# Kernel optimization log

Hardware: AMD Instinct MI355X
Metric: run time of the kernel (lower is better)

Reference implementation:

```python
import jax, jax.numpy as jnp
import numpy as np

D = 1024   # hidden
H = 4      # heads
HD = D // H
E = 8      # experts
FF = 4096  # expert ffn dim
CAP_FACTOR = 1.0


def _ln(x, g, b, eps=1e-5):
    mu = jnp.mean(x, -1, keepdims=True)
    v = jnp.mean((x - mu) ** 2, -1, keepdims=True)
    return (x - mu) * jax.lax.rsqrt(v + eps) * g + b


def setup_inputs() -> dict:
    key = jax.random.key(0)
    ks = jax.random.split(key, 8)
    L, N = 1024, 16
    s = 0.02
    return {
        "x": jax.random.normal(ks[0], (L, N, D), jnp.float32),
        "in_proj_w": jax.random.normal(ks[1], (3 * D, D), jnp.float32) * s,
        "in_proj_b": jnp.zeros((3 * D,), jnp.float32),
        "out_proj_w": jax.random.normal(ks[2], (D, D), jnp.float32) * s,
        "out_proj_b": jnp.zeros((D,), jnp.float32),
        "ln1_g": jnp.ones((D,), jnp.float32),
        "ln1_b": jnp.zeros((D,), jnp.float32),
        "ln2_g": jnp.ones((D,), jnp.float32),
        "ln2_b": jnp.zeros((D,), jnp.float32),
        "wg": jax.random.normal(ks[3], (D, E), jnp.float32) * s,
        "w1": jax.random.normal(ks[4], (E, D, FF), jnp.float32) * s,
        "b1": jnp.zeros((E, FF), jnp.float32),
        "w2": jax.random.normal(ks[5], (E, FF, D), jnp.float32) * s,
        "b2": jnp.zeros((E, D), jnp.float32),
    }


def _mha(x, w, b, ow, ob):
    # x: [L, N, D] (torch MultiheadAttention layout, batch_first=False)
    L, N, _ = x.shape
    qkv = x @ w.T + b
    q, k, v = jnp.split(qkv, 3, axis=-1)
    rh = lambda t: t.reshape(L, N, H, HD).transpose(1, 2, 0, 3)  # -> [N,H,L,HD]
    q, k, v = rh(q), rh(k), rh(v)
    scores = jnp.einsum('nhld,nhmd->nhlm', q, k) / np.float32(np.sqrt(HD))
    attn = jax.nn.softmax(scores, axis=-1)
    o = jnp.einsum('nhlm,nhmd->nhld', attn, v).transpose(2, 0, 1, 3).reshape(L, N, D)
    return o @ ow.T + ob


def _moe(x, wg, w1, b1, w2, b2):
    # top-1 switch gating with capacity drop, dispatch, grouped GEMM, combine
    L, N, _ = x.shape
    S = L * N
    cap = int(CAP_FACTOR * S) // E  # 2048
    xf = x.reshape(S, D)
    gates = jax.nn.softmax(xf @ wg, axis=-1)           # [S,E]
    idx = jnp.argmax(gates, axis=-1)                    # [S] top-1 expert
    mask1 = jax.nn.one_hot(idx, E, dtype=x.dtype)       # [S,E]
    # position of each token within its expert's queue
    loc = jnp.sum((jnp.cumsum(mask1, 0) - 1.0) * mask1, -1).astype(jnp.int32)
    keep = loc < cap                                    # capacity drop mask
    gate_val = jnp.take_along_axis(gates, idx[:, None], -1)[:, 0]
    slot = jnp.where(keep, idx.astype(jnp.int32) * cap + loc, E * cap)  # OOB if dropped
    disp = jnp.zeros((E * cap, D), x.dtype).at[slot].set(xf, mode='drop')
    disp = disp.reshape(E, cap, D)
    # expert = Linear(D,FF) -> Linear(FF,D), NO activation between (per source)
    h = jnp.einsum('ecd,edf->ecf', disp, w1) + b1[:, None, :]
    y = (jnp.einsum('ecf,efd->ecd', h, w2) + b2[:, None, :]).reshape(E * cap, D)
    out = jnp.where(keep[:, None], gate_val[:, None] * y[jnp.minimum(slot, E * cap - 1)], 0.0)
    return out.reshape(L, N, D)


def reference(x, in_proj_w, in_proj_b, out_proj_w, out_proj_b,
              ln1_g, ln1_b, ln2_g, ln2_b, wg, w1, b1, w2, b2):
    y1 = _ln(x + _mha(x, in_proj_w, in_proj_b, out_proj_w, out_proj_b), ln1_g, ln1_b)
    y2 = _ln(y1 + _moe(y1, wg, w1, b1, w2, b2), ln2_g, ln2_b)
    return y2
```

## Files before the change

### kernel.cpp

```cpp
#include <hip/hip_runtime.h>
#include <hip/hip_bf16.h>

typedef __bf16 bf16_t;
typedef bf16_t bf16x4 __attribute__((ext_vector_type(4)));
typedef bf16_t bf16x8 __attribute__((ext_vector_type(8)));
typedef float  f32x4  __attribute__((ext_vector_type(4)));
typedef _Float16 half4 __attribute__((ext_vector_type(4)));
typedef _Float16 half8 __attribute__((ext_vector_type(8)));

#define L_  1024
#define N_  16
#define S_  16384
#define D_  1024
#define H_  4
#define HD_ 256
#define E_  8
#define FF_ 4096
#define CAP_ 2048
#define ESLOTS_ (E_*CAP_)
#define TAU_ 0.03f

__device__ __forceinline__ void gload16(const void* g, void* l) {
  __builtin_amdgcn_global_load_lds(
      (const __attribute__((address_space(1))) void*)g,
      (__attribute__((address_space(3))) void*)l,
      16, 0, 0);
}

#define SRC_SWZ(lane) (((lane) & 3) ^ (((lane) >> 3) & 3))

__global__ __launch_bounds__(256) void split2(
    const float* __restrict__ in, _Float16* __restrict__ oh,
    _Float16* __restrict__ ol, long n4)
{
  long i = (long)blockIdx.x * blockDim.x + threadIdx.x;
  long stride = (long)gridDim.x * blockDim.x;
  for (; i < n4; i += stride) {
    float4 v = ((const float4*)in)[i];
    half4 h, l;
    h.x = (_Float16)v.x; l.x = (_Float16)((v.x - (float)h.x) * 4096.0f);
    h.y = (_Float16)v.y; l.y = (_Float16)((v.y - (float)h.y) * 4096.0f);
    h.z = (_Float16)v.z; l.z = (_Float16)((v.z - (float)h.z) * 4096.0f);
    h.w = (_Float16)v.w; l.w = (_Float16)((v.w - (float)h.w) * 4096.0f);
    ((half4*)oh)[i] = h;
    ((half4*)ol)[i] = l;
  }
}

template<int EPI, bool HAS_BIAS, int PROD>
__global__ __launch_bounds__(256) void hgemm3s(
    const _Float16* __restrict__ Ah, const _Float16* __restrict__ Al,
    const _Float16* __restrict__ Bh, const _Float16* __restrict__ Bl,
    float* __restrict__ Cf, _Float16* __restrict__ Ch, _Float16* __restrict__ Cl,
    const float* __restrict__ bias,
    int K, long lda, long ldb, long ldcf, long ldch,
    int Z2, long sA1, long sA2, long sB1, long sB2, long sC1, long sC2, long sBias)
{
  constexpr int NL = (PROD == 3) ? 2 : 1;
  __shared__ _Float16 tA[NL][2][128 * 32];
  __shared__ _Float16 tB[NL][2][64 * 32];
  const int z  = blockIdx.z;
  const int z1 = z / Z2, z2 = z - z1 * Z2;
  const long aoff = (long)z1 * sA1 + (long)z2 * sA2;
  const long boff = (long)z1 * sB1 + (long)z2 * sB2;
  const long coff = (long)z1 * sC1 + (long)z2 * sC2;
  const int brow = blockIdx.y * 128, bcol = blockIdx.x * 64;
  const int tid = threadIdx.x, lane = tid & 63, wid = tid >> 6;
  const int wr = (wid >> 1) * 64, wc = (wid & 1) * 32;
  const int fr = lane & 15;
  const int fqs = (((lane >> 4) ^ ((fr >> 1) & 3)) * 8);

  const bool isA = (wid < 2);
  int limb, dstoff, nch;
  const _Float16* ssrc;
  if constexpr (PROD == 3) {
    limb = wid & 1; nch = isA ? 8 : 4; dstoff = 0;
    ssrc = (wid == 0) ? Ah : (wid == 1) ? Al : (wid == 2) ? Bh : Bl;
  } else {
    limb = 0; nch = isA ? 4 : 2; dstoff = (wid & 1) * nch;
    ssrc = isA ? Ah : Bh;
  }
  const long sld = isA ? lda : ldb;
  const long soff = isA ? aoff : boff;
  int srow = (isA ? brow : bcol) + (lane >> 2);
  if constexpr (PROD == 1) srow += (wid & 1) * (isA ? 64 : 32);
  const _Float16* sbase = ssrc + soff + (long)srow * sld + SRC_SWZ(lane) * 8;

  f32x4 acc0[4][2], acc1[4][2];
#pragma unroll
  for (int mi = 0; mi < 4; ++mi)
#pragma unroll
    for (int ni = 0; ni < 2; ++ni) {
      acc0[mi][ni] = f32x4{0.f, 0.f, 0.f, 0.f};
      acc1[mi][ni] = f32x4{0.f, 0.f, 0.f, 0.f};
    }

  {
    _Float16* d0 = (isA ? &tA[limb][0][0] : &tB[limb][0][0]) + dstoff * 512;
    for (int i = 0; i < nch; ++i)
      gload16(sbase + (long)(16 * i) * sld, d0 + i * 512);
  }
  __syncthreads();

  const int NT = K >> 5;
  for (int t = 0; t < NT; ++t) {
    const int cur = t & 1;
    if (t + 1 < NT) {
      const int k1 = (t + 1) * 32;
      _Float16* d0 = (isA ? &tA[limb][cur ^ 1][0] : &tB[limb][cur ^ 1][0]) + dstoff * 512;
      for (int i = 0; i < nch; ++i)
        gload16(sbase + (long)(16 * i) * sld + k1, d0 + i * 512);
    }

    half8 bh_[2], bl_[2];
#pragma unroll
    for (int ni = 0; ni < 2; ++ni) {
      bh_[ni] = *(const half8*)&tB[0][cur][(wc + ni * 16 + fr) * 32 + fqs];
      if constexpr (PROD == 3)
        bl_[ni] = *(const half8*)&tB[1][cur][(wc + ni * 16 + fr) * 32 + fqs];
    }
    half8 ah_[4], al_[4];
#pragma unroll
    for (int mi = 0; mi < 4; ++mi) {
      ah_[mi] = *(const half8*)&tA[0][cur][(wr + mi * 16 + fr) * 32 + fqs];
      if constexpr (PROD == 3)
        al_[mi] = *(const half8*)&tA[1][cur][(wr + mi * 16 + fr) * 32 + fqs];
    }
#pragma unroll
    for (int mi = 0; mi < 4; ++mi)
#pragma unroll
      for (int ni = 0; ni < 2; ++ni)
        acc0[mi][ni] = __builtin_amdgcn_mfma_f32_16x16x32_f16(ah_[mi], bh_[ni], acc0[mi][ni], 0, 0, 0);
    if constexpr (PROD == 3) {
#pragma unroll
      for (int mi = 0; mi < 4; ++mi)
#pragma unroll
        for (int ni = 0; ni < 2; ++ni)
          acc1[mi][ni] = __builtin_amdgcn_mfma_f32_16x16x32_f16(ah_[mi], bl_[ni], acc1[mi][ni], 0, 0, 0);
#pragma unroll
      for (int mi = 0; mi < 4; ++mi)
#pragma unroll
        for (int ni = 0; ni < 2; ++ni)
          acc1[mi][ni] = __builtin_amdgcn_mfma_f32_16x16x32_f16(al_[mi], bh_[ni], acc1[mi][ni], 0, 0, 0);
    }
    __syncthreads();
  }

#pragma unroll
  for (int mi = 0; mi < 4; ++mi) {
#pragma unroll
    for (int ni = 0; ni < 2; ++ni) {
      int gcol = bcol + wc + ni * 16 + fr;
      float bv = 0.0f;
      if constexpr (HAS_BIAS) bv = bias[(long)z1 * sBias + gcol];
#pragma unroll
      for (int v = 0; v < 4; ++v) {
        int grow = brow + wr + mi * 16 + (lane >> 4) * 4 + v;
        float val = acc0[mi][ni][v] + bv;
        if constexpr (PROD == 3) val += acc1[mi][ni][v] * 0.000244140625f;
        if constexpr (EPI == 0) {
          Cf[coff + (long)grow * ldcf + gcol] = val;
        } else if constexpr (EPI == 1) {
          _Float16 hh = (_Float16)val;
          _Float16 ll = (_Float16)((val - (float)hh) * 4096.0f);
          long ci = coff + (long)grow * ldch + gcol;
          Ch[ci] = hh; Cl[ci] = ll;
        } else if constexpr (EPI == 3) {
          Ch[coff + (long)grow * ldch + gcol] = (_Float16)val;
        } else {
          if (bcol < 2048) {
            _Float16 hh = (_Float16)val;
            _Float16 ll = (_Float16)((val - (float)hh) * 4096.0f);
            long ci = (long)grow * ldch + gcol;
            Ch[ci] = hh; Cl[ci] = ll;
          } else {
            Cf[(long)grow * ldcf + (gcol - 2048)] = val;
          }
        }
      }
    }
  }
}

template<bool OUT_BF16, bool HAS_BIAS>
__global__ __launch_bounds__(256) void bgemm16(
    const bf16_t* __restrict__ A, const bf16_t* __restrict__ B,
    void* __restrict__ Cout, const float* __restrict__ bias,
    int K, long lda, long ldb, long ldc,
    long sA1, long sB1, long sC1, long sBias)
{
  __shared__ bf16_t tiles[2][2][128 * 32];
  const int z = blockIdx.z;
  const long coff = (long)z * sC1;
  const int brow = blockIdx.y * 128, bcol = blockIdx.x * 128;
  const int tid = threadIdx.x, lane = tid & 63, wid = tid >> 6;
  const int wr = (wid >> 1) * 64, wc = (wid & 1) * 64;
  const int fr = lane & 15;
  const int fqs = (((lane >> 4) ^ ((fr >> 1) & 3)) * 8);

  const bf16_t* src0 = (wid < 2) ? (A + (long)z * sA1) : (B + (long)z * sB1);
  const long ld = (wid < 2) ? lda : ldb;
  const int  rb = ((wid < 2) ? brow : bcol) + 64 * (wid & 1) + (lane >> 2);
  const bf16_t* srcbase = src0 + (long)rb * ld + SRC_SWZ(lane) * 8;
  const int tsel = wid >> 1, halfsel = wid & 1;

  f32x4 acc[4][4];
#pragma unroll
  for (int mi = 0; mi < 4; ++mi)
#pragma unroll
    for (int ni = 0; ni < 4; ++ni)
      acc[mi][ni] = f32x4{0.0f, 0.0f, 0.0f, 0.0f};

#pragma unroll
  for (int i = 0; i < 4; ++i)
    gload16(srcbase + (long)(16 * i) * ld, &tiles[tsel][0][(4 * halfsel + i) * 512]);
  __syncthreads();

  const int NT = K >> 5;
  for (int t = 0; t < NT; ++t) {
    const int cur = t & 1;
    if (t + 1 < NT) {
      const int k1 = (t + 1) * 32;
#pragma unroll
      for (int i = 0; i < 4; ++i)
        gload16(srcbase + (long)(16 * i) * ld + k1, &tiles[tsel][cur ^ 1][(4 * halfsel + i) * 512]);
    }
    bf16x8 af[4], bfv[4];
#pragma unroll
    for (int i = 0; i < 4; ++i) {
      af[i]  = *(const bf16x8*)&tiles[0][cur][(wr + i * 16 + fr) * 32 + fqs];
      bfv[i] = *(const bf16x8*)&tiles[1][cur][(wc + i * 16 + fr) * 32 + fqs];
    }
#pragma unroll
    for (int mi = 0; mi < 4; ++mi)
#pragma unroll
      for (int ni = 0; ni < 4; ++ni)
        acc[mi][ni] = __builtin_amdgcn_mfma_f32_16x16x32_bf16(af[mi], bfv[ni], acc[mi][ni], 0, 0, 0);
    __syncthreads();
  }

#pragma unroll
  for (int mi = 0; mi < 4; ++mi) {
#pragma unroll
    for (int ni = 0; ni < 4; ++ni) {
      int gcol = bcol + wc + ni * 16 + fr;
      float bv = 0.0f;
      if constexpr (HAS_BIAS) bv = bias[(long)z * sBias + gcol];
#pragma unroll
      for (int v = 0; v < 4; ++v) {
        int grow = brow + wr + mi * 16 + (lane >> 4) * 4 + v;
        float val = acc[mi][ni][v] + bv;
        long ci = coff + (long)grow * ldc + gcol;
        if constexpr (OUT_BF16) ((bf16_t*)Cout)[ci] = (bf16_t)val;
        else                    ((float*)Cout)[ci]  = val;
      }
    }
  }
}

template<typename TOUT>
__global__ __launch_bounds__(256) void transpose_f32(
    const float* __restrict__ src, TOUT* __restrict__ dst,
    long ld_src, long ld_dst, int Z2,
    long ss1, long ss2, long sd1, long sd2)
{
  __shared__ float t[32][33];
  const int z = blockIdx.z, z1 = z / Z2, z2 = z - z1 * Z2;
  src += (long)z1 * ss1 + (long)z2 * ss2;
  dst += (long)z1 * sd1 + (long)z2 * sd2;
  const int c0 = blockIdx.x * 32, r0 = blockIdx.y * 32;
  const int tx = threadIdx.x & 31, ty = threadIdx.x >> 5;
#pragma unroll
  for (int i = 0; i < 4; ++i)
    t[ty + i * 8][tx] = src[(long)(r0 + ty + i * 8) * ld_src + c0 + tx];
  __syncthreads();
#pragma unroll
  for (int i = 0; i < 4; ++i)
    dst[(long)(c0 + ty + i * 8) * ld_dst + r0 + tx] = (TOUT)t[tx][ty + i * 8];
}

__global__ __launch_bounds__(256) void transpose_split(
    const float* __restrict__ src, _Float16* __restrict__ dh, _Float16* __restrict__ dl,
    long ld_src, long ld_dst, int Z2,
    long ss1, long ss2, long sd1, long sd2)
{
  __shared__ float t[32][33];
  const int z = blockIdx.z, z1 = z / Z2, z2 = z - z1 * Z2;
  src += (long)z1 * ss1 + (long)z2 * ss2;
  dh  += (long)z1 * sd1 + (long)z2 * sd2;
  dl  += (long)z1 * sd1 + (long)z2 * sd2;
  const int c0 = blockIdx.x * 32, r0 = blockIdx.y * 32;
  const int tx = threadIdx.x & 31, ty = threadIdx.x >> 5;
#pragma unroll
  for (int i = 0; i < 4; ++i)
    t[ty + i * 8][tx] = src[(long)(r0 + ty + i * 8) * ld_src + c0 + tx];
  __syncthreads();
#pragma unroll
  for (int i = 0; i < 4; ++i) {
    float v = t[tx][ty + i * 8];
    _Float16 h = (_Float16)v;
    _Float16 l = (_Float16)((v - (float)h) * 4096.0f);
    long idx = (long)(c0 + ty + i * 8) * ld_dst + r0 + tx;
    dh[idx] = h;
    dl[idx] = l;
  }
}

template<bool WRITE_LO>
__global__ __launch_bounds__(256) void softmax_pack(
    float* __restrict__ Sm, float scale)
{
  __shared__ float red[4];
  const long row = blockIdx.x;
  const float4* p = (const float4*)(Sm + row * 1024);
  const int tid = threadIdx.x;
  float4 v = p[tid];
  float m = fmaxf(fmaxf(v.x, v.y), fmaxf(v.z, v.w));
#pragma unroll
  for (int o = 32; o; o >>= 1) m = fmaxf(m, __shfl_xor(m, o, 64));
  if ((tid & 63) == 0) red[tid >> 6] = m;
  __syncthreads();
  m = fmaxf(fmaxf(red[0], red[1]), fmaxf(red[2], red[3]));
  __syncthreads();
  float e0 = __expf((v.x - m) * scale);
  float e1 = __expf((v.y - m) * scale);
  float e2 = __expf((v.z - m) * scale);
  float e3 = __expf((v.w - m) * scale);
  float s = e0 + e1 + e2 + e3;
#pragma unroll
  for (int o = 32; o; o >>= 1) s += __shfl_xor(s, o, 64);
  if ((tid & 63) == 0) red[tid >> 6] = s;
  __syncthreads();
  s = red[0] + red[1] + red[2] + red[3];
  float inv = 1.0f / s;
  float p0 = e0 * inv, p1 = e1 * inv, p2 = e2 * inv, p3 = e3 * inv;
  half4 h;
  h.x = (_Float16)p0; h.y = (_Float16)p1; h.z = (_Float16)p2; h.w = (_Float16)p3;
  _Float16* base = (_Float16*)Sm + row * 2048;
  ((half4*)base)[tid] = h;
  if constexpr (WRITE_LO) {
    half4 l;
    l.x = (_Float16)((p0 - (float)h.x) * 4096.0f);
    l.y = (_Float16)((p1 - (float)h.y) * 4096.0f);
    l.z = (_Float16)((p2 - (float)h.z) * 4096.0f);
    l.w = (_Float16)((p3 - (float)h.w) * 4096.0f);
    ((half4*)(base + 1024))[tid] = l;
  }
}

__global__ __launch_bounds__(256) void add_ln_gate(
    const float* __restrict__ x, const float* __restrict__ attn,
    const float* __restrict__ g, const float* __restrict__ be,
    const float* __restrict__ wg, bf16_t* __restrict__ yb,
    int* __restrict__ idx, float* __restrict__ gval,
    int* __restrict__ bcnt16, int* __restrict__ blist16)
{
  __shared__ float red[4];
  __shared__ float lred[4][8];
  const long s = blockIdx.x;
  const int tid = threadIdx.x;
  const int lane = tid & 63, w = tid >> 6;
  float4 va = ((const float4*)(x + s * 1024))[tid];
  float4 vb = ((const float4*)(attn + s * 1024))[tid];
  float v0 = va.x + vb.x, v1 = va.y + vb.y, v2 = va.z + vb.z, v3 = va.w + vb.w;
  float sum = v0 + v1 + v2 + v3;
#pragma unroll
  for (int o = 32; o; o >>= 1) sum += __shfl_xor(sum, o, 64);
  if (lane == 0) red[w] = sum;
  __syncthreads();
  float mu = (red[0] + red[1] + red[2] + red[3]) * (1.0f / 1024.0f);
  __syncthreads();
  float d0 = v0 - mu, d1 = v1 - mu, d2 = v2 - mu, d3 = v3 - mu;
  float ss = d0 * d0 + d1 * d1 + d2 * d2 + d3 * d3;
#pragma unroll
  for (int o = 32; o; o >>= 1) ss += __shfl_xor(ss, o, 64);
  if (lane == 0) red[w] = ss;
  __syncthreads();
  float var = (red[0] + red[1] + red[2] + red[3]) * (1.0f / 1024.0f);
  float rstd = rsqrtf(var + 1e-5f);
  float4 vg  = ((const float4*)g)[tid];
  float4 vbe = ((const float4*)be)[tid];
  float y0 = d0 * rstd * vg.x + vbe.x;
  float y1v = d1 * rstd * vg.y + vbe.y;
  float y2v = d2 * rstd * vg.z + vbe.z;
  float y3 = d3 * rstd * vg.w + vbe.w;
  bf16x4 ov = { (bf16_t)y0, (bf16_t)y1v, (bf16_t)y2v, (bf16_t)y3 };
  *(bf16x4*)(yb + s * 1024 + tid * 4) = ov;
  float lg[8];
  const float* w0 = wg + (long)(tid * 4) * 8;
#pragma unroll
  for (int e = 0; e < 8; ++e)
    lg[e] = y0 * w0[e] + y1v * w0[8 + e] + y2v * w0[16 + e] + y3 * w0[24 + e];
#pragma unroll
  for (int e = 0; e < 8; ++e) {
#pragma unroll
    for (int o = 32; o; o >>= 1) lg[e] += __shfl_xor(lg[e], o, 64);
  }
  if (lane == 0) {
#pragma unroll
    for (int e = 0; e < 8; ++e) lred[w][e] = lg[e];
  }
  __syncthreads();
  if (tid == 0) {
    float Lg[8];
#pragma unroll
    for (int e = 0; e < 8; ++e)
      Lg[e] = lred[0][e] + lred[1][e] + lred[2][e] + lred[3][e];
    float best = Lg[0], second = -1e30f; int bi = 0;
#pragma unroll
    for (int e = 1; e < 8; ++e) {
      if (Lg[e] > best) { second = best; best = Lg[e]; bi = e; }
      else if (Lg[e] > second) second = Lg[e];
    }
    float sm = 0.0f;
#pragma unroll
    for (int e = 0; e < 8; ++e) sm += __expf(Lg[e] - best);
    idx[s] = bi;
    gval[s] = 1.0f / sm;
    if (best - second < TAU_) {
      int n = (int)(s & 15);
      int p = atomicAdd(&bcnt16[n], 1);
      if (p < 128) blist16[n * 128 + p] = (int)s;
    }
  }
}

__global__ void zero16(int* __restrict__ p)
{
  if (threadIdx.x < 16) p[threadIdx.x] = 0;
}

__global__ __launch_bounds__(64) void qp_gather(
    const int* __restrict__ bcnt16, const int* __restrict__ blist16,
    const _Float16* __restrict__ QKh, const _Float16* __restrict__ QKl,
    _Float16* __restrict__ Qph, _Float16* __restrict__ Qpl)
{
  const int b = blockIdx.x;
  const int n = b >> 7, p = b & 127;
  const int t = threadIdx.x;
  half8* dh = (half8*)(Qph + (long)b * 1024);
  half8* dl = (half8*)(Qpl + (long)b * 1024);
  int cnt = bcnt16[n]; if (cnt > 128) cnt = 128;
  if (p < cnt) {
    long srow = (long)blist16[b] * 2048;
    const half8* sh = (const half8*)(QKh + srow);
    const half8* sl = (const half8*)(QKl + srow);
    dh[t * 2]     = sh[t * 2];
    dh[t * 2 + 1] = sh[t * 2 + 1];
    dl[t * 2]     = sl[t * 2];
    dl[t * 2 + 1] = sl[t * 2 + 1];
  } else {
    half8 z;
#pragma unroll
    for (int i = 0; i < 8; ++i) z[i] = (_Float16)0.0f;
    dh[t * 2] = z; dh[t * 2 + 1] = z;
    dl[t * 2] = z; dl[t * 2 + 1] = z;
  }
}

__global__ __launch_bounds__(256) void gate_fix(
    const int* __restrict__ bcnt16, const int* __restrict__ blist16,
    const float* __restrict__ attn_p, const float* __restrict__ x,
    const float* __restrict__ g, const float* __restrict__ be,
    const float* __restrict__ wg,
    int* __restrict__ idx, float* __restrict__ gval)
{
  const int b = blockIdx.x;
  const int n = b >> 7, p = b & 127;
  int cnt = bcnt16[n]; if (cnt > 128) cnt = 128;
  if (p >= cnt) return;
  const long s = blist16[b];
  __shared__ float red[4];
  __shared__ float lred[4][8];
  const int tid = threadIdx.x;
  const int lane = tid & 63, w = tid >> 6;
  float4 va = ((const float4*)(x + s * 1024))[tid];
  float4 vb = ((const float4*)(attn_p + (long)b * 1024))[tid];
  float v0 = va.x + vb.x, v1 = va.y + vb.y, v2 = va.z + vb.z, v3 = va.w + vb.w;
  float sum = v0 + v1 + v2 + v3;
#pragma unroll
  for (int o = 32; o; o >>= 1) sum += __shfl_xor(sum, o, 64);
  if (lane == 0) red[w] = sum;
  __syncthreads();
  float mu = (red[0] + red[1] + red[2] + red[3]) * (1.0f / 1024.0f);
  __syncthreads();
  float d0 = v0 - mu, d1 = v1 - mu, d2 = v2 - mu, d3 = v3 - mu;
  float ss = d0 * d0 + d1 * d1 + d2 * d2 + d3 * d3;
#pragma unroll
  for (int o = 32; o; o >>= 1) ss += __shfl_xor(ss, o, 64);
  if (lane == 0) red[w] = ss;
  __syncthreads();
  float var = (red[0] + red[1] + red[2] + red[3]) * (1.0f / 1024.0f);
  float rstd = rsqrtf(var + 1e-5f);
  float4 vg  = ((const float4*)g)[tid];
  float4 vbe = ((const float4*)be)[tid];
  float y0 = d0 * rstd * vg.x + vbe.x;
  float y1v = d1 * rstd * vg.y + vbe.y;
  float y2v = d2 * rstd * vg.z + vbe.z;
  float y3 = d3 * rstd * vg.w + vbe.w;
  float lg[8];
  const float* w0 = wg + (long)(tid * 4) * 8;
#pragma unroll
  for (int e = 0; e < 8; ++e)
    lg[e] = y0 * w0[e] + y1v * w0[8 + e] + y2v * w0[16 + e] + y3 * w0[24 + e];
#pragma unroll
  for (int e = 0; e < 8; ++e) {
#pragma unroll
    for (int o = 32; o; o >>= 1) lg[e] += __shfl_xor(lg[e], o, 64);
  }
  if (lane == 0) {
#pragma unroll
    for (int e = 0; e < 8; ++e) lred[w][e] = lg[e];
  }
  __syncthreads();
  if (tid == 0) {
    float Lg[8];
#pragma unroll
    for (int e = 0; e < 8; ++e)
      Lg[e] = lred[0][e] + lred[1][e] + lred[2][e] + lred[3][e];
    float best = Lg[0]; int bi = 0;
#pragma unroll
    for (int e = 1; e < 8; ++e) { if (Lg[e] > best) { best = Lg[e]; bi = e; } }
    float sm = 0.0f;
#pragma unroll
    for (int e = 0; e < 8; ++e) sm += __expf(Lg[e] - best);
    idx[s] = bi;
    gval[s] = 1.0f / sm;
  }
}

__global__ __launch_bounds__(256) void combine_ln(
    const bf16_t* __restrict__ y1b, const bf16_t* __restrict__ ymoe,
    const int* __restrict__ slot, const float* __restrict__ gval,
    const float* __restrict__ g, const float* __restrict__ be,
    float* __restrict__ out)
{
  __shared__ float red[4];
  const long s = blockIdx.x;
  const int tid = threadIdx.x;
  const int lane = tid & 63, w = tid >> 6;
  int sl = slot[s];
  bool keep = sl < ESLOTS_;
  float gv = keep ? gval[s] : 0.0f;
  long mrow = keep ? (long)sl * 1024 : 0;
  bf16x4 ya = *(const bf16x4*)(y1b + s * 1024 + tid * 4);
  bf16x4 ym = *(const bf16x4*)(ymoe + mrow + tid * 4);
  float v0 = (float)ya[0] + gv * (float)ym[0];
  float v1 = (float)ya[1] + gv * (float)ym[1];
  float v2 = (float)ya[2] + gv * (float)ym[2];
  float v3 = (float)ya[3] + gv * (float)ym[3];
  float sum = v0 + v1 + v2 + v3;
#pragma unroll
  for (int o = 32; o; o >>= 1) sum += __shfl_xor(sum, o, 64);
  if (lane == 0) red[w] = sum;
  __syncthreads();
  float mu = (red[0] + red[1] + red[2] + red[3]) * (1.0f / 1024.0f);
  __syncthreads();
  float d0 = v0 - mu, d1 = v1 - mu, d2 = v2 - mu, d3 = v3 - mu;
  float ss = d0 * d0 + d1 * d1 + d2 * d2 + d3 * d3;
#pragma unroll
  for (int o = 32; o; o >>= 1) ss += __shfl_xor(ss, o, 64);
  if (lane == 0) red[w] = ss;
  __syncthreads();
  float var = (red[0] + red[1] + red[2] + red[3]) * (1.0f / 1024.0f);
  float rstd = rsqrtf(var + 1e-5f);
  float4 vg  = ((const float4*)g)[tid];
  float4 vbe = ((const float4*)be)[tid];
  float4 ov = {d0 * rstd * vg.x + vbe.x, d1 * rstd * vg.y + vbe.y,
               d2 * rstd * vg.z + vbe.z, d3 * rstd * vg.w + vbe.w};
  ((float4*)(out + s * 1024))[tid] = ov;
}

__global__ __launch_bounds__(1024) void route_scan(
    const int* __restrict__ idx, int* __restrict__ slot, int* __restrict__ tfs)
{
  __shared__ int c_lds[8][1024];
  const int tid = threadIdx.x;
  const int lane = tid & 63, wid = tid >> 6;

  for (int j = tid; j < ESLOTS_; j += 1024) tfs[j] = -1;

  int myc[8] = {0, 0, 0, 0, 0, 0, 0, 0};
  for (int j = 0; j < 16; ++j) {
    int e = idx[tid * 16 + j];
    myc[e]++;
  }
#pragma unroll
  for (int e = 0; e < 8; ++e) c_lds[e][tid] = myc[e];
  __syncthreads();

  if (wid < 8) {
    int carry = 0;
    for (int cb = 0; cb < 1024; cb += 64) {
      int v = c_lds[wid][cb + lane];
#pragma unroll
      for (int o = 1; o < 64; o <<= 1) {
        int t = __shfl_up(v, o, 64);
        if (lane >= o) v += t;
      }
      v += carry;
      c_lds[wid][cb + lane] = v;
      carry = __shfl(v, 63, 64);
    }
  }
  __syncthreads();

  int run[8] = {0, 0, 0, 0, 0, 0, 0, 0};
  for (int j = 0; j < 16; ++j) {
    int s = tid * 16 + j;
    int e = idx[s];
    int excl = c_lds[e][tid] - myc[e];
    int loc = excl + run[e];
    run[e]++;
    int sl = (loc < CAP_) ? e * CAP_ + loc : ESLOTS_;
    slot[s] = sl;
    if (sl < ESLOTS_) tfs[sl] = s;
  }
}

__global__ void dispatch_rows(
    const int* __restrict__ tfs, const bf16_t* __restrict__ y1b,
    bf16_t* __restrict__ disp)
{
  const int row = blockIdx.x;
  const int t = tfs[row];
  bf16x8* d = (bf16x8*)(disp + (long)row * 1024);
  if (t >= 0) {
    const bf16x8* sp = (const bf16x8*)(y1b + (long)t * 1024);
    d[threadIdx.x] = sp[threadIdx.x];
  } else {
    bf16x8 zv;
#pragma unroll
    for (int i = 0; i < 8; ++i) zv[i] = (bf16_t)0.0f;
    d[threadIdx.x] = zv;
  }
}

__global__ void fill_val(float* __restrict__ p, float v, long n)
{
  long i = (long)blockIdx.x * blockDim.x + threadIdx.x;
  long stride = (long)gridDim.x * blockDim.x;
  for (; i < n; i += stride) p[i] = v;
}

extern "C" void kernel_launch(void* const* d_in, const int* in_sizes, int n_in,
                              void* d_out, int out_size, void* d_ws, size_t ws_size,
                              hipStream_t stream)
{
  const float* x    = (const float*)d_in[0];
  const float* Wqkv = (const float*)d_in[1];
  const float* bqkv = (const float*)d_in[2];
  const float* Wo   = (const float*)d_in[3];
  const float* bo   = (const float*)d_in[4];
  const float* g1   = (const float*)d_in[5];
  const float* b1n  = (const float*)d_in[6];
  const float* g2   = (const float*)d_in[7];
  const float* b2n  = (const float*)d_in[8];
  const float* wg   = (const float*)d_in[9];
  const float* w1   = (const float*)d_in[10];
  const float* b1e  = (const float*)d_in[11];
  const float* w2   = (const float*)d_in[12];
  const float* b2e  = (const float*)d_in[13];
  float* out = (float*)d_out;

  const size_t MB = 1ull << 20;
  const size_t REQUIRED = 384 * MB;
  if (ws_size < REQUIRED) {
    fill_val<<<2048, 256, 0, stream>>>(out, (float)(ws_size >> 20), (long)out_size);
    return;
  }

  char* ws = (char*)d_ws;
  _Float16* Xh   = (_Float16*)(ws + 0);
  _Float16* Xl   = (_Float16*)(ws + 32 * MB);
  _Float16* Wqh  = (_Float16*)(ws + 64 * MB);
  _Float16* Wql  = (_Float16*)(ws + 70 * MB);
  float*    scores = (float*)(ws + 0);
  _Float16* Woh  = (_Float16*)(ws + 64 * MB);
  _Float16* Wol  = (_Float16*)(ws + 66 * MB);
  _Float16* QKh  = (_Float16*)(ws + 80 * MB);
  _Float16* QKl  = (_Float16*)(ws + 144 * MB);
  float*    Vf32 = (float*)(ws + 208 * MB);
  _Float16* oh   = (_Float16*)(ws + 208 * MB);
  _Float16* vTh  = (_Float16*)(ws + 272 * MB);
  _Float16* vTl  = (_Float16*)(ws + 304 * MB);
  float*    attn = (float*)(ws + 0);
  bf16_t*   y1b  = (bf16_t*)(ws + 208 * MB);
  float*    scp   = (float*)(ws + 0);
  _Float16* Qph   = (_Float16*)(ws + 32 * MB);
  _Float16* Qpl   = (_Float16*)(ws + 36 * MB);
  _Float16* o_ph  = (_Float16*)(ws + 40 * MB);
  _Float16* o_pl  = (_Float16*)(ws + 44 * MB);
  float*    attnp = (float*)(ws + 48 * MB);
  int*      idx  = (int*)(ws + 336 * MB);
  int*      slot = idx + S_;
  float*    gval = (float*)(slot + S_);
  int*      tfs  = (int*)(gval + S_);
  int*      bcnt16  = tfs + S_;
  int*      blist16 = bcnt16 + 16;
  bf16_t*   disp = (bf16_t*)(ws + 272 * MB);
  bf16_t*   W1t  = (bf16_t*)(ws + 0);
  bf16_t*   W2t  = (bf16_t*)(ws + 0);
  bf16_t*   h    = (bf16_t*)(ws + 80 * MB);
  bf16_t*   ymoe = (bf16_t*)(ws + 304 * MB);

  zero16<<<1, 64, 0, stream>>>(bcnt16);

  split2<<<4096, 256, 0, stream>>>(x, Xh, Xl, (long)S_ * D_ / 4);
  split2<<<2048, 256, 0, stream>>>(Wqkv, Wqh, Wql, (long)3 * D_ * D_ / 4);

  hgemm3s<2, true, 3><<<dim3(48, 128, 1), 256, 0, stream>>>(
      Xh, Xl, Wqh, Wql, Vf32, QKh, QKl, bqkv,
      D_, D_, D_, D_, 2 * D_,
      1, 0, 0, 0, 0, 0, 0, 0);

  split2<<<1024, 256, 0, stream>>>(Wo, Woh, Wol, (long)D_ * D_ / 4);

  transpose_split<<<dim3(HD_ / 32, L_ / 32, 64), 256, 0, stream>>>(
      Vf32, vTh, vTl, (long)N_ * D_, L_,
      H_, D_, HD_, (long)H_ * HD_ * L_, (long)HD_ * L_);

  for (int g = 0; g < 4; ++g) {
    const long qko = (long)g * 4 * 2048;
    hgemm3s<0, false, 1><<<dim3(16, 8, 16), 256, 0, stream>>>(
        QKh + qko, QKl + qko, QKh + qko + 1024, QKl + qko + 1024,
        scores, nullptr, nullptr, nullptr,
        HD_, (long)N_ * 2048, (long)N_ * 2048, L_, 0,
        H_, 2048, 256, 2048, 256, (long)H_ * L_ * L_, (long)L_ * L_, 0);
    softmax_pack<false><<<4 * H_ * L_, 256, 0, stream>>>(scores, 0.0625f);
    hgemm3s<3, false, 1><<<dim3(4, 8, 16), 256, 0, stream>>>(
        (_Float16*)scores, (_Float16*)scores + 1024,
        vTh + (long)g * 4 * H_ * HD_ * L_, vTl + (long)g * 4 * H_ * HD_ * L_,
        nullptr, oh + (long)g * 4 * D_, nullptr, nullptr,
        L_, 2048, L_, 0, (long)N_ * D_,
        H_, (long)4 * L_ * 2048, (long)L_ * 2048,
        (long)H_ * HD_ * L_, (long)HD_ * L_, D_, HD_, 0);
  }

  hgemm3s<0, true, 1><<<dim3(16, 128, 1), 256, 0, stream>>>(
      oh, nullptr, Woh, Wol, attn, nullptr, nullptr, bo,
      D_, D_, D_, D_, 0,
      1, 0, 0, 0, 0, 0, 0, 0);

  add_ln_gate<<<S_, 256, 0, stream>>>(x, attn, g1, b1n, wg, y1b,
                                      idx, gval, bcnt16, blist16);

  qp_gather<<<2048, 64, 0, stream>>>(bcnt16, blist16, QKh, QKl, Qph, Qpl);
  hgemm3s<0, false, 3><<<dim3(16, 1, 64), 256, 0, stream>>>(
      Qph, Qpl, QKh + 1024, QKl + 1024, scp, nullptr, nullptr, nullptr,
      HD_, 1024, (long)N_ * 2048, 1024, 0,
      4, (long)128 * 1024, 256, 2048, 256,
      (long)4 * 128 * 1024, (long)128 * 1024, 0);
  softmax_pack<true><<<64 * 128, 256, 0, stream>>>(scp, 0.0625f);
  hgemm3s<1, false, 3><<<dim3(4, 1, 64), 256, 0, stream>>>(
      (_Float16*)scp, (_Float16*)scp + 1024, vTh, vTl,
      nullptr, o_ph, o_pl, nullptr,
      L_, 2048, L_, 0, 1024,
      4, (long)4 * 128 * 2048, (long)128 * 2048,
      (long)H_ * HD_ * L_, (long)HD_ * L_,
      (long)128 * 1024, 256, 0);
  hgemm3s<0, true, 3><<<dim3(16, 16, 1), 256, 0, stream>>>(
      o_ph, o_pl, Woh, Wol, attnp, nullptr, nullptr, bo,
      D_, D_, D_, D_, 0,
      1, 0, 0, 0, 0, 0, 0, 0);
  gate_fix<<<2048, 256, 0, stream>>>(bcnt16, blist16, attnp, x,
                                     g1, b1n, wg, idx, gval);

  route_scan<<<1, 1024, 0, stream>>>(idx, slot, tfs);

  dispatch_rows<<<ESLOTS_, 128, 0, stream>>>(tfs, y1b, disp);

  transpose_f32<bf16_t><<<dim3(FF_ / 32, D_ / 32, E_), 256, 0, stream>>>(
      w1, W1t, FF_, D_, 1, (long)D_ * FF_, 0, (long)FF_ * D_, 0);

  bgemm16<true, true><<<dim3(32, 16, 8), 256, 0, stream>>>(
      disp, W1t, h, b1e, D_, D_, D_, FF_,
      (long)CAP_ * D_, (long)FF_ * D_, (long)CAP_ * FF_, FF_);

  transpose_f32<bf16_t><<<dim3(D_ / 32, FF_ / 32, E_), 256, 0, stream>>>(
      w2, W2t, D_, FF_, 1, (long)FF_ * D_, 0, (long)D_ * FF_, 0);

  bgemm16<true, true><<<dim3(8, 16, 8), 256, 0, stream>>>(
      h, W2t, ymoe, b2e, FF_, FF_, FF_, D_,
      (long)CAP_ * FF_, (long)D_ * FF_, (long)CAP_ * D_, D_);

  combine_ln<<<S_, 256, 0, stream>>>(y1b, ymoe, slot, gval, g2, b2n, out);
}
```

Baseline: 1.610 ms.

## Use 256x128 MoE GEMM tiles and single-fp16 attention scores with fewer passes

The expert GEMM kernel now uses 512-thread blocks covering 256x128 output tiles. Each warp loads three 16-row chunks into separate A and B shared tiles, so more output is computed per B-tile load. Attention scores are now written directly as fp16 by the QK GEMM and normalised in place by a new fp16 softmax. The PV GEMM then reads only the high half, not a hi/lo split pair. Batches double to cut the loop to two groups, which lowers score memory traffic and launch count at some cost in precision of the attention probabilities.

```diff
diff --git a/kernel.cpp b/kernel.cpp
--- a/kernel.cpp
+++ b/kernel.cpp
@@ -183,26 +183,41 @@
 }
 
 template<bool OUT_BF16, bool HAS_BIAS>
-__global__ __launch_bounds__(256) void bgemm16(
+__global__ __launch_bounds__(512) void bgemm256(
     const bf16_t* __restrict__ A, const bf16_t* __restrict__ B,
     void* __restrict__ Cout, const float* __restrict__ bias,
     int K, long lda, long ldb, long ldc,
     long sA1, long sB1, long sC1, long sBias)
 {
-  __shared__ bf16_t tiles[2][2][128 * 32];
+  __shared__ bf16_t tA[2][256 * 32];
+  __shared__ bf16_t tB[2][128 * 32];
   const int z = blockIdx.z;
   const long coff = (long)z * sC1;
-  const int brow = blockIdx.y * 128, bcol = blockIdx.x * 128;
+  const int brow = blockIdx.y * 256, bcol = blockIdx.x * 128;
   const int tid = threadIdx.x, lane = tid & 63, wid = tid >> 6;
   const int wr = (wid >> 1) * 64, wc = (wid & 1) * 64;
   const int fr = lane & 15;
   const int fqs = (((lane >> 4) ^ ((fr >> 1) & 3)) * 8);
 
-  const bf16_t* src0 = (wid < 2) ? (A + (long)z * sA1) : (B + (long)z * sB1);
-  const long ld = (wid < 2) ? lda : ldb;
-  const int  rb = ((wid < 2) ? brow : bcol) + 64 * (wid & 1) + (lane >> 2);
-  const bf16_t* srcbase = src0 + (long)rb * ld + SRC_SWZ(lane) * 8;
-  const int tsel = wid >> 1, halfsel = wid & 1;
+  const bf16_t* Ab = A + (long)z * sA1;
+  const bf16_t* Bb = B + (long)z * sB1;
+
+  const bf16_t* csrc[3];
+  bf16_t* cd0[3];
+  bf16_t* cd1[3];
+  long cld[3];
+#pragma unroll
+  for (int i = 0; i < 3; ++i) {
+    int c = wid * 3 + i;
+    bool cA = c < 16;
+    const bf16_t* s0 = cA ? Ab : Bb;
+    long ld = cA ? lda : ldb;
+    int r0 = cA ? (brow + 16 * c) : (bcol + 16 * (c - 16));
+    csrc[i] = s0 + (long)(r0 + (lane >> 2)) * ld + SRC_SWZ(lane) * 8;
+    cld[i] = ld;
+    cd0[i] = cA ? &tA[0][c * 512] : &tB[0][(c - 16) * 512];
+    cd1[i] = cA ? &tA[1][c * 512] : &tB[1][(c - 16) * 512];
+  }
 
   f32x4 acc[4][4];
 #pragma unroll
@@ -212,8 +227,7 @@
       acc[mi][ni] = f32x4{0.0f, 0.0f, 0.0f, 0.0f};
 
 #pragma unroll
-  for (int i = 0; i < 4; ++i)
-    gload16(srcbase + (long)(16 * i) * ld, &tiles[tsel][0][(4 * halfsel + i) * 512]);
+  for (int i = 0; i < 3; ++i) gload16(csrc[i], cd0[i]);
   __syncthreads();
 
   const int NT = K >> 5;
@@ -222,14 +236,14 @@
     if (t + 1 < NT) {
       const int k1 = (t + 1) * 32;
 #pragma unroll
-      for (int i = 0; i < 4; ++i)
-        gload16(srcbase + (long)(16 * i) * ld + k1, &tiles[tsel][cur ^ 1][(4 * halfsel + i) * 512]);
+      for (int i = 0; i < 3; ++i)
+        gload16(csrc[i] + k1, cur ? cd0[i] : cd1[i]);
     }
     bf16x8 af[4], bfv[4];
 #pragma unroll
     for (int i = 0; i < 4; ++i) {
-      af[i]  = *(const bf16x8*)&tiles[0][cur][(wr + i * 16 + fr) * 32 + fqs];
-      bfv[i] = *(const bf16x8*)&tiles[1][cur][(wc + i * 16 + fr) * 32 + fqs];
+      af[i]  = *(const bf16x8*)&tA[cur][(wr + i * 16 + fr) * 32 + fqs];
+      bfv[i] = *(const bf16x8*)&tB[cur][(wc + i * 16 + fr) * 32 + fqs];
     }
 #pragma unroll
     for (int mi = 0; mi < 4; ++mi)
@@ -304,6 +318,39 @@
     dh[idx] = h;
     dl[idx] = l;
   }
+}
+
+__global__ __launch_bounds__(256) void softmax16(
+    _Float16* __restrict__ Sm, float scale)
+{
+  __shared__ float red[4];
+  const long row = blockIdx.x;
+  half4* p = (half4*)(Sm + row * 1024);
+  const int tid = threadIdx.x;
+  half4 hv = p[tid];
+  float v0 = (float)hv.x, v1 = (float)hv.y, v2 = (float)hv.z, v3 = (float)hv.w;
+  float m = fmaxf(fmaxf(v0, v1), fmaxf(v2, v3));
+#pragma unroll
+  for (int o = 32; o; o >>= 1) m = fmaxf(m, __shfl_xor(m, o, 64));
+  if ((tid & 63) == 0) red[tid >> 6] = m;
+  __syncthreads();
+  m = fmaxf(fmaxf(red[0], red[1]), fmaxf(red[2], red[3]));
+  __syncthreads();
+  float e0 = __expf((v0 - m) * scale);
+  float e1 = __expf((v1 - m) * scale);
+  float e2 = __expf((v2 - m) * scale);
+  float e3 = __expf((v3 - m) * scale);
+  float s = e0 + e1 + e2 + e3;
+#pragma unroll
+  for (int o = 32; o; o >>= 1) s += __shfl_xor(s, o, 64);
+  if ((tid & 63) == 0) red[tid >> 6] = s;
+  __syncthreads();
+  s = red[0] + red[1] + red[2] + red[3];
+  float inv = 1.0f / s;
+  half4 w;
+  w.x = (_Float16)(e0 * inv); w.y = (_Float16)(e1 * inv);
+  w.z = (_Float16)(e2 * inv); w.w = (_Float16)(e3 * inv);
+  p[tid] = w;
 }
 
 template<bool WRITE_LO>
@@ -675,7 +722,7 @@
   _Float16* Xl   = (_Float16*)(ws + 32 * MB);
   _Float16* Wqh  = (_Float16*)(ws + 64 * MB);
   _Float16* Wql  = (_Float16*)(ws + 70 * MB);
-  float*    scores = (float*)(ws + 0);
+  _Float16* scores16 = (_Float16*)(ws + 0);
   _Float16* Woh  = (_Float16*)(ws + 64 * MB);
   _Float16* Wol  = (_Float16*)(ws + 66 * MB);
   _Float16* QKh  = (_Float16*)(ws + 80 * MB);
@@ -720,20 +767,20 @@
       Vf32, vTh, vTl, (long)N_ * D_, L_,
       H_, D_, HD_, (long)H_ * HD_ * L_, (long)HD_ * L_);
 
-  for (int g = 0; g < 4; ++g) {
-    const long qko = (long)g * 4 * 2048;
-    hgemm3s<0, false, 1><<<dim3(16, 8, 16), 256, 0, stream>>>(
+  for (int g = 0; g < 2; ++g) {
+    const long qko = (long)g * 8 * 2048;
+    hgemm3s<3, false, 1><<<dim3(16, 8, 32), 256, 0, stream>>>(
         QKh + qko, QKl + qko, QKh + qko + 1024, QKl + qko + 1024,
-        scores, nullptr, nullptr, nullptr,
-        HD_, (long)N_ * 2048, (long)N_ * 2048, L_, 0,
+        nullptr, scores16, nullptr, nullptr,
+        HD_, (long)N_ * 2048, (long)N_ * 2048, 0, L_,
         H_, 2048, 256, 2048, 256, (long)H_ * L_ * L_, (long)L_ * L_, 0);
-    softmax_pack<false><<<4 * H_ * L_, 256, 0, stream>>>(scores, 0.0625f);
-    hgemm3s<3, false, 1><<<dim3(4, 8, 16), 256, 0, stream>>>(
-        (_Float16*)scores, (_Float16*)scores + 1024,
-        vTh + (long)g * 4 * H_ * HD_ * L_, vTl + (long)g * 4 * H_ * HD_ * L_,
-        nullptr, oh + (long)g * 4 * D_, nullptr, nullptr,
-        L_, 2048, L_, 0, (long)N_ * D_,
-        H_, (long)4 * L_ * 2048, (long)L_ * 2048,
+    softmax16<<<8 * H_ * L_, 256, 0, stream>>>(scores16, 0.0625f);
+    hgemm3s<3, false, 1><<<dim3(4, 8, 32), 256, 0, stream>>>(
+        scores16, nullptr,
+        vTh + (long)g * 8 * H_ * HD_ * L_, vTl + (long)g * 8 * H_ * HD_ * L_,
+        nullptr, oh + (long)g * 8 * D_, nullptr, nullptr,
+        L_, L_, L_, 0, (long)N_ * D_,
+        H_, (long)H_ * L_ * L_, (long)L_ * L_,
         (long)H_ * HD_ * L_, (long)HD_ * L_, D_, HD_, 0);
   }
 
@@ -773,14 +820,14 @@
   transpose_f32<bf16_t><<<dim3(FF_ / 32, D_ / 32, E_), 256, 0, stream>>>(
       w1, W1t, FF_, D_, 1, (long)D_ * FF_, 0, (long)FF_ * D_, 0);
 
-  bgemm16<true, true><<<dim3(32, 16, 8), 256, 0, stream>>>(
+  bgemm256<true, true><<<dim3(32, 8, 8), 512, 0, stream>>>(
       disp, W1t, h, b1e, D_, D_, D_, FF_,
       (long)CAP_ * D_, (long)FF_ * D_, (long)CAP_ * FF_, FF_);
 
   transpose_f32<bf16_t><<<dim3(D_ / 32, FF_ / 32, E_), 256, 0, stream>>>(
       w2, W2t, D_, FF_, 1, (long)FF_ * D_, 0, (long)D_ * FF_, 0);
 
-  bgemm16<true, true><<<dim3(8, 16, 8), 256, 0, stream>>>(
+  bgemm256<true, true><<<dim3(8, 8, 8), 512, 0, stream>>>(
       h, W2t, ymoe, b2e, FF_, FF_, FF_, D_,
       (long)CAP_ * FF_, (long)D_ * FF_, (long)CAP_ * D_, D_);
 
```

After: 1.588 ms. Within noise of the previous version (-1.3%).
